# Kernel tuning notes

Hardware: AMD Instinct MI355X
Metric: run time of the kernel (lower is better)

## Reference

```python
import jax, jax.numpy as jnp
import numpy as np

B, N, D_IN, D_OUT = 4096, 200, 64, 64


def setup_inputs() -> dict:
    key = jax.random.key(0)
    k1, k2 = jax.random.split(key)
    x = jax.random.normal(k1, (B, N, D_IN), dtype=jnp.float32)
    # weight initialized like TF add_weight default (glorot-ish scale via normal here)
    weight = jax.random.normal(k2, (1, N, D_IN, D_OUT), dtype=jnp.float32) * (1.0 / np.sqrt(D_IN))
    bias = jnp.zeros((1, N, D_OUT), dtype=jnp.float32)
    return {"x": x, "weight": weight, "bias": bias}


def reference(x, weight, bias):
    # Original: (x[..., None] * weight).sum(-2) + bias
    # == per-token matmul: out[b,n,o] = sum_i x[b,n,i] * weight[0,n,i,o] + bias[0,n,o]
    out = jnp.einsum('bni,nio->bno', x, weight[0])
    return out + bias
```

## Files before the change

kernel.cpp:

```cpp
#include <hip/hip_runtime.h>


#define B_DIM 4096
#define N_DIM 200
#define D 64
#define ROWS_PER_BLOCK 128
#define CHUNK 32
#define NWAVES 4
#define ROWS_PER_WAVE (CHUNK / NWAVES)

__global__ __launch_bounds__(256, 4)
void nlinear_kernel(const float* __restrict__ x,
                    const float* __restrict__ w,
                    const float* __restrict__ bias,
                    float* __restrict__ out) {
    const int n    = blockIdx.y;
    const int b0   = blockIdx.x * ROWS_PER_BLOCK;
    const int tid  = threadIdx.x;
    const int lane = tid & 63;
    const int wave = tid >> 6;

    __shared__ float x_lds[CHUNK][D];

    const float* wn = w + (size_t)n * (D * D);
    float wreg[D];
#pragma unroll
    for (int i = 0; i < D; ++i) wreg[i] = wn[i * D + lane];

    const float bv = bias[n * D + lane];

    const size_t row_stride = (size_t)N_DIM * D;
    const float* xb = x   + (size_t)b0 * row_stride + (size_t)n * D;
    float*       ob = out + (size_t)b0 * row_stride + (size_t)n * D;

    for (int c0 = 0; c0 < ROWS_PER_BLOCK; c0 += CHUNK) {
#pragma unroll
        for (int k = 0; k < 2; ++k) {
            const int idx = tid + k * 256;
            const int r   = idx >> 4;
            const int f   = (idx & 15) << 2;
            const float4 v = *(const float4*)(xb + (size_t)(c0 + r) * row_stride + f);
            *(float4*)(&x_lds[r][f]) = v;
        }
        __syncthreads();

#pragma unroll
        for (int rr = 0; rr < ROWS_PER_WAVE; ++rr) {
            const int r = wave * ROWS_PER_WAVE + rr;
            const float* xr = &x_lds[r][0];
            float a0 = 0.f, a1 = 0.f, a2 = 0.f, a3 = 0.f;
#pragma unroll
            for (int i = 0; i < D; i += 16) {
                const float4 v0 = *(const float4*)(xr + i);
                const float4 v1 = *(const float4*)(xr + i + 4);
                const float4 v2 = *(const float4*)(xr + i + 8);
                const float4 v3 = *(const float4*)(xr + i + 12);
                a0 = fmaf(v0.x, wreg[i + 0], a0);
                a0 = fmaf(v0.y, wreg[i + 1], a0);
                a0 = fmaf(v0.z, wreg[i + 2], a0);
                a0 = fmaf(v0.w, wreg[i + 3], a0);
                a1 = fmaf(v1.x, wreg[i + 4], a1);
                a1 = fmaf(v1.y, wreg[i + 5], a1);
                a1 = fmaf(v1.z, wreg[i + 6], a1);
                a1 = fmaf(v1.w, wreg[i + 7], a1);
                a2 = fmaf(v2.x, wreg[i + 8], a2);
                a2 = fmaf(v2.y, wreg[i + 9], a2);
                a2 = fmaf(v2.z, wreg[i + 10], a2);
                a2 = fmaf(v2.w, wreg[i + 11], a2);
                a3 = fmaf(v3.x, wreg[i + 12], a3);
                a3 = fmaf(v3.y, wreg[i + 13], a3);
                a3 = fmaf(v3.z, wreg[i + 14], a3);
                a3 = fmaf(v3.w, wreg[i + 15], a3);
            }
            ob[(size_t)(c0 + r) * row_stride + lane] = ((a0 + a1) + (a2 + a3)) + bv;
        }
        __syncthreads();
    }
}

extern "C" void kernel_launch(void* const* d_in, const int* in_sizes, int n_in,
                              void* d_out, int out_size, void* d_ws, size_t ws_size,
                              hipStream_t stream) {
    const float* x    = (const float*)d_in[0];
    const float* w    = (const float*)d_in[1];
    const float* bias = (const float*)d_in[2];
    float*       out  = (float*)d_out;

    dim3 grid(B_DIM / ROWS_PER_BLOCK, N_DIM);
    nlinear_kernel<<<grid, dim3(256), 0, stream>>>(x, w, bias, out);
}
```

Measured before the change: 438.8 us.

## Load x rows via wave-uniform scalar loads instead of LDS staging

Drops the shared-memory staging and block barriers. Each wave now owns 64 consecutive batch rows and reads every x row through a wave-uniform pointer (readfirstlane), so the compiler can use scalar loads that broadcast the row to all lanes. Each block covers 256 rows, which halves the grid, and the bias is folded into the accumulator's starting value. The scalar path removes LDS traffic and synchronisation, but each wave's x reads become serialized scalar loads with less memory-level parallelism, and fewer blocks may hurt latency hiding.

```diff
diff --git a/kernel.cpp b/kernel.cpp
--- a/kernel.cpp
+++ b/kernel.cpp
@@ -4,10 +4,17 @@
 #define B_DIM 4096
 #define N_DIM 200
 #define D 64
-#define ROWS_PER_BLOCK 128
-#define CHUNK 32
-#define NWAVES 4
-#define ROWS_PER_WAVE (CHUNK / NWAVES)
+#define ROWS_PER_WAVE 64
+#define ROWS_PER_BLOCK 256
+
+typedef __attribute__((ext_vector_type(16))) float f32x16;
+
+__device__ __forceinline__ const float* uniform_ptr(const float* p) {
+    uint64_t v = (uint64_t)(uintptr_t)p;
+    uint32_t lo = __builtin_amdgcn_readfirstlane((uint32_t)v);
+    uint32_t hi = __builtin_amdgcn_readfirstlane((uint32_t)(v >> 32));
+    return (const float*)(uintptr_t)(((uint64_t)hi << 32) | lo);
+}
 
 __global__ __launch_bounds__(256, 4)
 void nlinear_kernel(const float* __restrict__ x,
@@ -15,12 +22,10 @@
                     const float* __restrict__ bias,
                     float* __restrict__ out) {
     const int n    = blockIdx.y;
-    const int b0   = blockIdx.x * ROWS_PER_BLOCK;
     const int tid  = threadIdx.x;
     const int lane = tid & 63;
-    const int wave = tid >> 6;
-
-    __shared__ float x_lds[CHUNK][D];
+    const int wave = __builtin_amdgcn_readfirstlane(tid >> 6);
+    const int b0   = blockIdx.x * ROWS_PER_BLOCK + wave * ROWS_PER_WAVE;
 
     const float* wn = w + (size_t)n * (D * D);
     float wreg[D];
@@ -30,51 +35,28 @@
     const float bv = bias[n * D + lane];
 
     const size_t row_stride = (size_t)N_DIM * D;
-    const float* xb = x   + (size_t)b0 * row_stride + (size_t)n * D;
-    float*       ob = out + (size_t)b0 * row_stride + (size_t)n * D;
+    const float* xrow = uniform_ptr(x + (size_t)b0 * row_stride + (size_t)n * D);
+    float*       orow = out + (size_t)b0 * row_stride + (size_t)n * D + lane;
 
-    for (int c0 = 0; c0 < ROWS_PER_BLOCK; c0 += CHUNK) {
+    for (int r = 0; r < ROWS_PER_WAVE; ++r) {
+        const f32x16* xv = (const f32x16*)xrow;
+        const f32x16 c0 = xv[0];
+        const f32x16 c1 = xv[1];
+        const f32x16 c2 = xv[2];
+        const f32x16 c3 = xv[3];
+
+        float a0 = bv, a1 = 0.f, a2 = 0.f, a3 = 0.f;
 #pragma unroll
-        for (int k = 0; k < 2; ++k) {
-            const int idx = tid + k * 256;
-            const int r   = idx >> 4;
-            const int f   = (idx & 15) << 2;
-            const float4 v = *(const float4*)(xb + (size_t)(c0 + r) * row_stride + f);
-            *(float4*)(&x_lds[r][f]) = v;
+        for (int j = 0; j < 16; ++j) {
+            a0 = fmaf(c0[j], wreg[j],      a0);
+            a1 = fmaf(c1[j], wreg[16 + j], a1);
+            a2 = fmaf(c2[j], wreg[32 + j], a2);
+            a3 = fmaf(c3[j], wreg[48 + j], a3);
         }
-        __syncthreads();
+        *orow = (a0 + a1) + (a2 + a3);
 
-#pragma unroll
-        for (int rr = 0; rr < ROWS_PER_WAVE; ++rr) {
-            const int r = wave * ROWS_PER_WAVE + rr;
-            const float* xr = &x_lds[r][0];
-            float a0 = 0.f, a1 = 0.f, a2 = 0.f, a3 = 0.f;
-#pragma unroll
-            for (int i = 0; i < D; i += 16) {
-                const float4 v0 = *(const float4*)(xr + i);
-                const float4 v1 = *(const float4*)(xr + i + 4);
-                const float4 v2 = *(const float4*)(xr + i + 8);
-                const float4 v3 = *(const float4*)(xr + i + 12);
-                a0 = fmaf(v0.x, wreg[i + 0], a0);
-                a0 = fmaf(v0.y, wreg[i + 1], a0);
-                a0 = fmaf(v0.z, wreg[i + 2], a0);
-                a0 = fmaf(v0.w, wreg[i + 3], a0);
-                a1 = fmaf(v1.x, wreg[i + 4], a1);
-                a1 = fmaf(v1.y, wreg[i + 5], a1);
-                a1 = fmaf(v1.z, wreg[i + 6], a1);
-                a1 = fmaf(v1.w, wreg[i + 7], a1);
-                a2 = fmaf(v2.x, wreg[i + 8], a2);
-                a2 = fmaf(v2.y, wreg[i + 9], a2);
-                a2 = fmaf(v2.z, wreg[i + 10], a2);
-                a2 = fmaf(v2.w, wreg[i + 11], a2);
-                a3 = fmaf(v3.x, wreg[i + 12], a3);
-                a3 = fmaf(v3.y, wreg[i + 13], a3);
-                a3 = fmaf(v3.z, wreg[i + 14], a3);
-                a3 = fmaf(v3.w, wreg[i + 15], a3);
-            }
-            ob[(size_t)(c0 + r) * row_stride + lane] = ((a0 + a1) + (a2 + a3)) + bv;
-        }
-        __syncthreads();
+        xrow += row_stride;
+        orow += row_stride;
     }
 }
 
```

Result: slower. 1.019 ms (+132.3%).
